# Performance work log

Measured on AMD Instinct MI355X. Metric: run time of the kernel, lower is better.

## Reference

```python
import jax, jax.numpy as jnp
import numpy as np

N_NODES = 50000
N_EDGES = 800000
IN_DIM = 128
HIDDEN = 64
NEG_SLOPE = 0.2


def setup_inputs() -> dict:
    key = jax.random.key(0)
    ks = jax.random.split(key, 8)
    x = jax.random.normal(ks[0], (N_NODES, IN_DIM), dtype=jnp.float32)
    edge_index = jax.random.randint(ks[1], (2, N_EDGES), 0, N_NODES, dtype=jnp.int64)
    # GATConv params (heads=1)
    W = jax.random.normal(ks[2], (HIDDEN, IN_DIM), dtype=jnp.float32) / np.sqrt(IN_DIM)
    att_src = jax.random.normal(ks[3], (HIDDEN,), dtype=jnp.float32) / np.sqrt(HIDDEN)
    att_dst = jax.random.normal(ks[4], (HIDDEN,), dtype=jnp.float32) / np.sqrt(HIDDEN)
    bias_conv = jnp.zeros((HIDDEN,), dtype=jnp.float32)
    # final Linear(hidden, 1)
    W_lin = jax.random.normal(ks[5], (1, HIDDEN), dtype=jnp.float32) / np.sqrt(HIDDEN)
    b_lin = jnp.zeros((1,), dtype=jnp.float32)
    return {"x": x, "edge_index": edge_index, "W": W, "att_src": att_src,
            "att_dst": att_dst, "bias_conv": bias_conv, "W_lin": W_lin, "b_lin": b_lin}


def _gat_forward(x, edge_index, W, att_src, att_dst, bias_conv, W_lin, b_lin):
    n = x.shape[0]
    # add self-loops (PyG GATConv default)
    loop = jnp.arange(n, dtype=edge_index.dtype)
    src = jnp.concatenate([edge_index[0], loop])  # source nodes j (messages from)
    dst = jnp.concatenate([edge_index[1], loop])  # destination nodes i (aggregated at)

    h = x @ W.T                                   # [N, H] projected features
    a_src = h @ att_src                           # [N]
    a_dst = h @ att_dst                           # [N]

    e = jax.nn.leaky_relu(a_src[src] + a_dst[dst], NEG_SLOPE)  # [E']
    # segment softmax over incoming edges of each destination node
    m = jax.ops.segment_max(e, dst, num_segments=n)            # [N]
    ex = jnp.exp(e - m[dst])
    s = jax.ops.segment_sum(ex, dst, num_segments=n)           # [N]
    alpha = ex / s[dst]                                        # [E']

    out = jax.ops.segment_sum(alpha[:, None] * h[src], dst, num_segments=n)
    out = out + bias_conv                         # [N, H]

    out = jax.nn.relu(out)
    # dropout p=0.5 is a no-op in eval mode
    y = jax.nn.sigmoid(out @ W_lin.T + b_lin)     # [N, 1]
    return y


def reference(x, edge_index, W, att_src, att_dst, bias_conv, W_lin, b_lin):
    return _gat_forward(x, edge_index, W, att_src, att_dst, bias_conv, W_lin, b_lin)
```

## Files before the change

kernel.cpp:

```cpp
#include <hip/hip_runtime.h>
#include <hip/hip_bf16.h>
#include <hip/hip_fp16.h>
#include <cstdint>

#define IND 128
#define HID 64
#define NEG_SLOPE 0.2f
#define EPB 4096
#define CBSHIFT 8
#define BCAP 8192
#define SORT_THREADS 256
#define EPT (EPB / SORT_THREADS)

__device__ __forceinline__ unsigned short f2bf_bits(float f) {
  __hip_bfloat16 b = __float2bfloat16(f);
  return *reinterpret_cast<unsigned short*>(&b);
}
__device__ __forceinline__ unsigned short f2h_bits(float f) {
  __half h = __float2half(f);
  return *reinterpret_cast<unsigned short*>(&h);
}
__device__ __forceinline__ float h2f_bits(unsigned short u) {
  __half_raw r; r.x = u;
  return __half2float(__half(r));
}
__device__ __forceinline__ float bf2f_bits(unsigned short u) {
  return __uint_as_float((unsigned)u << 16);
}
__device__ __forceinline__ unsigned pack_bf2(float lo, float hi) {
  return (unsigned)f2bf_bits(lo) | ((unsigned)f2bf_bits(hi) << 16);
}
__device__ __forceinline__ float bf_lo(unsigned u) {
  return __uint_as_float(u << 16);
}
__device__ __forceinline__ float bf_hi(unsigned u) {
  return __uint_as_float(u & 0xFFFF0000u);
}

__global__ __launch_bounds__(256) void k_proj_sort(
    const float* __restrict__ x, const float* __restrict__ W,
    const float* __restrict__ att_s, const float* __restrict__ att_d,
    unsigned short* __restrict__ h, float* __restrict__ a_src,
    float* __restrict__ a_dst,
    const int* __restrict__ ei, int* __restrict__ gcur,
    unsigned* __restrict__ tmp, int E, long long E2,
    int nSort, int nbuck, int n)
{
  __shared__ __align__(16) char smem[49664];
  const int tid = threadIdx.x;

  if (blockIdx.x < (unsigned)nSort) {
    int* hist       = (int*)smem;
    int* sums       = hist + 256;
    int* cur        = sums + 256;
    int* gbase      = cur + 256;
    unsigned* sorted = (unsigned*)(gbase + 256);

    hist[tid] = 0;
    __syncthreads();

    const long long i0 = (long long)blockIdx.x * EPB;

    unsigned pk[EPT];
#pragma unroll
    for (int j = 0; j < EPT; ++j) {
      long long idx = i0 + j * SORT_THREADS + tid;
      unsigned v = 0xFFFFFFFFu;
      if (idx < E2) {
        int s, d;
        if (idx < E) { s = ei[idx]; d = ei[E + idx]; }
        else         { s = d = (int)(idx - E); }
        v = ((unsigned)d << 16) | (unsigned)s;
        atomicAdd(&hist[d >> CBSHIFT], 1);
      }
      pk[j] = v;
    }
    __syncthreads();

    sums[tid] = hist[tid];
    __syncthreads();
    for (int off = 1; off < 256; off <<= 1) {
      int t = (tid >= off) ? sums[tid - off] : 0;
      __syncthreads();
      sums[tid] += t;
      __syncthreads();
    }
    {
      const int lstart_t = sums[tid] - hist[tid];
      cur[tid] = lstart_t;
      gbase[tid] = (tid < nbuck && hist[tid] > 0)
                     ? tid * BCAP + atomicAdd(&gcur[tid], hist[tid]) : 0;
    }
    __syncthreads();
    hist[tid] = sums[tid] - hist[tid];
    __syncthreads();

#pragma unroll
    for (int j = 0; j < EPT; ++j) {
      unsigned v = pk[j];
      if (v != 0xFFFFFFFFu) {
        int b = v >> (16 + CBSHIFT);
        int lpos = atomicAdd(&cur[b], 1);
        sorted[lpos] = v;
      }
    }
    __syncthreads();

    const int cntE = (int)((E2 - i0 < EPB) ? (E2 - i0) : EPB);
    for (int i = tid; i < cntE; i += SORT_THREADS) {
      unsigned v = sorted[i];
      int b = v >> (16 + CBSHIFT);
      tmp[gbase[b] + (i - hist[b])] = v;
    }
    return;
  }

  float*    xs   = (float*)smem;
  unsigned* wt   = (unsigned*)(smem + 32768);
  float*    sa_l = (float*)(smem + 49152);
  float*    sd_l = (float*)(smem + 49408);

  const int nodeBase = (blockIdx.x - nSort) * 64;

  if (tid < 64) { sa_l[tid] = 0.f; sd_l[tid] = 0.f; }

#pragma unroll
  for (int it = 0; it < 4; ++it) {
    int fi = (it * 256 + tid) * 8;
    int row = fi >> 7, k = fi & 127;
    float4 w0 = *(const float4*)(W + fi);
    float4 w1 = *(const float4*)(W + fi + 4);
    uint4 pv;
    pv.x = pack_bf2(w0.x, w0.y);
    pv.y = pack_bf2(w0.z, w0.w);
    pv.z = pack_bf2(w1.x, w1.y);
    pv.w = pack_bf2(w1.z, w1.w);
    int c = (k >> 3) ^ ((row >> 2) & 7);
    ((uint4*)wt)[row * 16 + c] = pv;
  }
#pragma unroll
  for (int it = 0; it < 8; ++it) {
    int fi = (it * 256 + tid) * 4;
    int nl = fi >> 7, k = fi & 127;
    int ks = k ^ (((nl >> 2) & 7) << 2);
    int node = nodeBase + nl; if (node >= n) node = n - 1;
    float4 v = *(const float4*)(x + (size_t)node * IND + k);
    *(float4*)&xs[nl * 128 + ks] = v;
  }
  __syncthreads();

  const int ng = tid & 15;
  const int hg = tid >> 4;
  const int swzA = (ng & 7) << 2;
  const int swzB = hg & 7;
  const float* xrow0 = &xs[(4 * ng) * 128];
  const uint4* wrow0 = ((const uint4*)wt) + (4 * hg) * 16;

  float acc[4][4];
#pragma unroll
  for (int j = 0; j < 4; ++j)
#pragma unroll
    for (int i = 0; i < 4; ++i) acc[j][i] = 0.f;

  for (int k = 0; k < IND; k += 8) {
    float4 a0[4], a1[4];
#pragma unroll
    for (int j = 0; j < 4; ++j) {
      a0[j] = *(const float4*)(xrow0 + j * 128 + (k ^ swzA));
      a1[j] = *(const float4*)(xrow0 + j * 128 + ((k + 4) ^ swzA));
    }
    uint4 bw[4];
#pragma unroll
    for (int i = 0; i < 4; ++i)
      bw[i] = wrow0[i * 16 + ((k >> 3) ^ swzB)];

#pragma unroll
    for (int i = 0; i < 4; ++i) {
      float b0 = bf_lo(bw[i].x), b1 = bf_hi(bw[i].x);
      float b2 = bf_lo(bw[i].y), b3 = bf_hi(bw[i].y);
      float b4 = bf_lo(bw[i].z), b5 = bf_hi(bw[i].z);
      float b6 = bf_lo(bw[i].w), b7 = bf_hi(bw[i].w);
#pragma unroll
      for (int j = 0; j < 4; ++j) {
        acc[j][i] = fmaf(a0[j].x, b0, acc[j][i]);
        acc[j][i] = fmaf(a0[j].y, b1, acc[j][i]);
        acc[j][i] = fmaf(a0[j].z, b2, acc[j][i]);
        acc[j][i] = fmaf(a0[j].w, b3, acc[j][i]);
        acc[j][i] = fmaf(a1[j].x, b4, acc[j][i]);
        acc[j][i] = fmaf(a1[j].y, b5, acc[j][i]);
        acc[j][i] = fmaf(a1[j].z, b6, acc[j][i]);
        acc[j][i] = fmaf(a1[j].w, b7, acc[j][i]);
      }
    }
  }

#pragma unroll
  for (int j = 0; j < 4; ++j) {
    int node = nodeBase + 4 * ng + j;
    if (node < n) {
      ushort4 hv;
      hv.x = f2bf_bits(acc[j][0]);
      hv.y = f2bf_bits(acc[j][1]);
      hv.z = f2bf_bits(acc[j][2]);
      hv.w = f2bf_bits(acc[j][3]);
      *(ushort4*)(h + (size_t)node * HID + 4 * hg) = hv;
    }
  }

  float4 as4 = *(const float4*)(att_s + 4 * hg);
  float4 ad4 = *(const float4*)(att_d + 4 * hg);
#pragma unroll
  for (int j = 0; j < 4; ++j) {
    float ps = acc[j][0]*as4.x + acc[j][1]*as4.y + acc[j][2]*as4.z + acc[j][3]*as4.w;
    float pd = acc[j][0]*ad4.x + acc[j][1]*ad4.y + acc[j][2]*ad4.z + acc[j][3]*ad4.w;
    ps += __shfl_xor(ps, 16, 64); ps += __shfl_xor(ps, 32, 64);
    pd += __shfl_xor(pd, 16, 64); pd += __shfl_xor(pd, 32, 64);
    if ((tid & 63) < 16) {
      atomicAdd(&sa_l[4 * ng + j], ps);
      atomicAdd(&sd_l[4 * ng + j], pd);
    }
  }
  __syncthreads();
  if (tid < 64) {
    int node = nodeBase + tid;
    if (node < n) { a_src[node] = sa_l[tid]; a_dst[node] = sd_l[tid]; }
  }
}

__global__ __launch_bounds__(1024) void k_csr(
    const unsigned* __restrict__ tmp, const int* __restrict__ gcur,
    const float* __restrict__ a_src, const float* __restrict__ a_dst,
    int* __restrict__ row_start, int* __restrict__ deg_out,
    unsigned* __restrict__ csr4, int n, int nbuck)
{
  __shared__ int degl[256], sums[256], cur[256];
  __shared__ float adl[256];

  const int tid = threadIdx.x;
  const int b   = blockIdx.x;
  const int n0  = b << CBSHIFT;
  const int base = b * BCAP;
  const int next = base + gcur[b];

  if (tid < 256) {
    degl[tid] = 0;
    const int node = n0 + tid;
    adl[tid] = (node < n) ? a_dst[node] : 0.f;
  }
  __syncthreads();

  for (int i = base + tid; i < next; i += 1024)
    atomicAdd(&degl[(tmp[i] >> 16) - n0], 1);
  __syncthreads();

  if (tid < 256) sums[tid] = degl[tid];
  __syncthreads();
  for (int off = 1; off < 256; off <<= 1) {
    int t = (tid >= off && tid < 256) ? sums[tid - off] : 0;
    __syncthreads();
    if (tid < 256) sums[tid] += t;
    __syncthreads();
  }
  if (tid < 256) {
    const int rs = base + sums[tid] - degl[tid];
    cur[tid] = rs;
    const int node = n0 + tid;
    if (node < n) { row_start[node] = rs; deg_out[node] = degl[tid]; }
  }
  __syncthreads();

  for (int i = base + tid; i < next; i += 1024) {
    unsigned v = tmp[i];
    int s  = (int)(v & 0xFFFFu);
    int dl = (int)(v >> 16) - n0;
    float sc = a_src[s] + adl[dl];
    sc = (sc >= 0.f) ? sc : NEG_SLOPE * sc;
    float w = expf(sc);
    int pos = atomicAdd(&cur[dl], 1);
    csr4[pos] = (unsigned)s | ((unsigned)f2h_bits(w) << 16);
  }
}

__global__ __launch_bounds__(256) void k_gather_final(
    const int* __restrict__ row_start, const int* __restrict__ deg,
    const unsigned* __restrict__ csr4, const unsigned short* __restrict__ h,
    const float* __restrict__ bias, const float* __restrict__ W_lin,
    const float* __restrict__ b_lin, float* __restrict__ y, int n)
{
  const int lane = threadIdx.x & 63;
  const int wid  = threadIdx.x >> 6;
  const int node = blockIdx.x * 4 + wid;
  if (node >= n) return;

  const int rs = row_start[node];
  const int dg = deg[node];

  const int quarter = lane >> 4;
  const int sub     = lane & 15;

  float wpart = 0.f;
  float acc0 = 0.f, acc1 = 0.f, acc2 = 0.f, acc3 = 0.f;

  for (int b = 0; b < dg; b += 64) {
    int i = b + lane;
    unsigned pk = (i < dg) ? csr4[rs + i] : 0u;
    wpart += h2f_bits((unsigned short)(pk >> 16));
    const int cnt = (dg - b < 64) ? (dg - b) : 64;

    int j = 0;
    for (; j + 8 <= cnt; j += 8) {
#pragma unroll
      for (int g = 0; g < 2; ++g) {
        int e = j + 4 * g + quarter;
        unsigned pe = __shfl(pk, e, 64);
        float we = h2f_bits((unsigned short)(pe >> 16));
        unsigned se = pe & 0xFFFFu;
        ushort4 hb = ((const ushort4*)(h + (size_t)se * HID))[sub];
        acc0 = fmaf(we, bf2f_bits(hb.x), acc0);
        acc1 = fmaf(we, bf2f_bits(hb.y), acc1);
        acc2 = fmaf(we, bf2f_bits(hb.z), acc2);
        acc3 = fmaf(we, bf2f_bits(hb.w), acc3);
      }
    }
    for (; j < cnt; j += 4) {
      int e = j + quarter;
      bool val = e < cnt;
      unsigned pe = __shfl(pk, val ? e : 0, 64);
      float we = val ? h2f_bits((unsigned short)(pe >> 16)) : 0.f;
      unsigned se = val ? (pe & 0xFFFFu) : 0u;
      ushort4 hb = ((const ushort4*)(h + (size_t)se * HID))[sub];
      acc0 = fmaf(we, bf2f_bits(hb.x), acc0);
      acc1 = fmaf(we, bf2f_bits(hb.y), acc1);
      acc2 = fmaf(we, bf2f_bits(hb.z), acc2);
      acc3 = fmaf(we, bf2f_bits(hb.w), acc3);
    }
  }

  acc0 += __shfl_xor(acc0, 16, 64); acc0 += __shfl_xor(acc0, 32, 64);
  acc1 += __shfl_xor(acc1, 16, 64); acc1 += __shfl_xor(acc1, 32, 64);
  acc2 += __shfl_xor(acc2, 16, 64); acc2 += __shfl_xor(acc2, 32, 64);
  acc3 += __shfl_xor(acc3, 16, 64); acc3 += __shfl_xor(acc3, 32, 64);

  float wsum = wpart;
#pragma unroll
  for (int o = 32; o; o >>= 1) wsum += __shfl_xor(wsum, o, 64);
  const float inv = 1.f / wsum;

  float4 bb = ((const float4*)bias)[sub];
  float4 ww = ((const float4*)W_lin)[sub];
  float v0 = fmaxf(acc0 * inv + bb.x, 0.f);
  float v1 = fmaxf(acc1 * inv + bb.y, 0.f);
  float v2 = fmaxf(acc2 * inv + bb.z, 0.f);
  float v3 = fmaxf(acc3 * inv + bb.w, 0.f);
  float z = v0 * ww.x + v1 * ww.y + v2 * ww.z + v3 * ww.w;
#pragma unroll
  for (int o = 8; o; o >>= 1) z += __shfl_xor(z, o, 64);
  if (lane == 0)
    y[node] = 1.f / (1.f + expf(-(z + b_lin[0])));
}


extern "C" void kernel_launch(void* const* d_in, const int* in_sizes, int n_in,
                              void* d_out, int out_size, void* d_ws, size_t ws_size,
                              hipStream_t stream)
{
  const float* x     = (const float*)d_in[0];
  const int*   ei    = (const int*)d_in[1];
  const float* W     = (const float*)d_in[2];
  const float* att_s = (const float*)d_in[3];
  const float* att_d = (const float*)d_in[4];
  const float* bias  = (const float*)d_in[5];
  const float* W_lin = (const float*)d_in[6];
  const float* b_lin = (const float*)d_in[7];
  float* y = (float*)d_out;

  const int n = in_sizes[0] / IND;
  const int E = in_sizes[1] / 2;
  const long long E2 = (long long)E + n;
  const int nSort = (int)((E2 + EPB - 1) / EPB);
  const int nProj = (n + 63) / 64;
  const int nbuck = (n + (1 << CBSHIFT) - 1) >> CBSHIFT;

  char* ws = (char*)d_ws;
  unsigned short* h = (unsigned short*)ws; ws += (size_t)n * HID * sizeof(unsigned short);
  float*    a_src  = (float*)ws;    ws += (size_t)n * sizeof(float);
  float*    a_dst  = (float*)ws;    ws += (size_t)n * sizeof(float);
  int*      row_st = (int*)ws;      ws += (size_t)n * sizeof(int);
  int*      deg    = (int*)ws;      ws += (size_t)n * sizeof(int);
  int*      gcur   = (int*)ws;      ws += (size_t)nbuck * sizeof(int);
  unsigned* tmp    = (unsigned*)ws; ws += (size_t)nbuck * BCAP * sizeof(unsigned);
  unsigned* csr4   = (unsigned*)ws; ws += (size_t)nbuck * BCAP * sizeof(unsigned);

  hipMemsetAsync(gcur, 0, (size_t)nbuck * sizeof(int), stream);

  k_proj_sort<<<nSort + nProj, 256, 0, stream>>>(
      x, W, att_s, att_d, h, a_src, a_dst,
      ei, gcur, tmp, E, E2, nSort, nbuck, n);

  k_csr<<<nbuck, 1024, 0, stream>>>(tmp, gcur, a_src, a_dst, row_st, deg, csr4,
                                    n, nbuck);

  k_gather_final<<<(n + 3) / 4, 256, 0, stream>>>(
      row_st, deg, csr4, h, bias, W_lin, b_lin, y, n);
}
```

Baseline: 141.0 us.

## Fuse CSR build and neighbor gather into one kernel using shared-memory CSR

Merges the CSR construction kernel and the gather/final kernel so each bucket block builds its CSR slice in LDS (32KB) and then its 16 waves process the bucket's 256 destination nodes directly. This removes the global csr4/row_start/deg writes and reads plus one kernel launch. In exchange, parallelism for the gather drops to nbuck (~196) blocks of 1024 threads with high LDS use, which may underfill the GPU during the latency-bound h gathers.

After: 147.0 us. 4.3% more time.

```diff
diff --git a/kernel.cpp b/kernel.cpp
--- a/kernel.cpp
+++ b/kernel.cpp
@@ -227,14 +227,16 @@
   }
 }
 
-__global__ __launch_bounds__(1024) void k_csr(
+__global__ __launch_bounds__(1024) void k_csr_gather(
     const unsigned* __restrict__ tmp, const int* __restrict__ gcur,
     const float* __restrict__ a_src, const float* __restrict__ a_dst,
-    int* __restrict__ row_start, int* __restrict__ deg_out,
-    unsigned* __restrict__ csr4, int n, int nbuck)
+    const unsigned short* __restrict__ h,
+    const float* __restrict__ bias, const float* __restrict__ W_lin,
+    const float* __restrict__ b_lin, float* __restrict__ y, int n)
 {
   __shared__ int degl[256], sums[256], cur[256];
   __shared__ float adl[256];
+  __shared__ unsigned csrw[BCAP];
 
   const int tid = threadIdx.x;
   const int b   = blockIdx.x;
@@ -261,12 +263,7 @@
     if (tid < 256) sums[tid] += t;
     __syncthreads();
   }
-  if (tid < 256) {
-    const int rs = base + sums[tid] - degl[tid];
-    cur[tid] = rs;
-    const int node = n0 + tid;
-    if (node < n) { row_start[node] = rs; deg_out[node] = degl[tid]; }
-  }
+  if (tid < 256) cur[tid] = sums[tid] - degl[tid];
   __syncthreads();
 
   for (int i = base + tid; i < next; i += 1024) {
@@ -277,44 +274,52 @@
     sc = (sc >= 0.f) ? sc : NEG_SLOPE * sc;
     float w = expf(sc);
     int pos = atomicAdd(&cur[dl], 1);
-    csr4[pos] = (unsigned)s | ((unsigned)f2h_bits(w) << 16);
-  }
-}
-
-__global__ __launch_bounds__(256) void k_gather_final(
-    const int* __restrict__ row_start, const int* __restrict__ deg,
-    const unsigned* __restrict__ csr4, const unsigned short* __restrict__ h,
-    const float* __restrict__ bias, const float* __restrict__ W_lin,
-    const float* __restrict__ b_lin, float* __restrict__ y, int n)
-{
-  const int lane = threadIdx.x & 63;
-  const int wid  = threadIdx.x >> 6;
-  const int node = blockIdx.x * 4 + wid;
-  if (node >= n) return;
-
-  const int rs = row_start[node];
-  const int dg = deg[node];
-
+    csrw[pos] = (unsigned)s | ((unsigned)f2h_bits(w) << 16);
+  }
+  __syncthreads();
+
+  const int lane    = tid & 63;
+  const int wid     = tid >> 6;
   const int quarter = lane >> 4;
   const int sub     = lane & 15;
 
-  float wpart = 0.f;
-  float acc0 = 0.f, acc1 = 0.f, acc2 = 0.f, acc3 = 0.f;
-
-  for (int b = 0; b < dg; b += 64) {
-    int i = b + lane;
-    unsigned pk = (i < dg) ? csr4[rs + i] : 0u;
-    wpart += h2f_bits((unsigned short)(pk >> 16));
-    const int cnt = (dg - b < 64) ? (dg - b) : 64;
-
-    int j = 0;
-    for (; j + 8 <= cnt; j += 8) {
-#pragma unroll
-      for (int g = 0; g < 2; ++g) {
-        int e = j + 4 * g + quarter;
-        unsigned pe = __shfl(pk, e, 64);
-        float we = h2f_bits((unsigned short)(pe >> 16));
-        unsigned se = pe & 0xFFFFu;
+  for (int nl = wid; nl < 256; nl += 16) {
+    const int node = n0 + nl;
+    if (node >= n) break;
+
+    const int dg  = degl[nl];
+    const int rsl = sums[nl] - dg;
+
+    float wpart = 0.f;
+    float acc0 = 0.f, acc1 = 0.f, acc2 = 0.f, acc3 = 0.f;
+
+    for (int bb = 0; bb < dg; bb += 64) {
+      int i = bb + lane;
+      unsigned pk = (i < dg) ? csrw[rsl + i] : 0u;
+      wpart += h2f_bits((unsigned short)(pk >> 16));
+      const int cnt = (dg - bb < 64) ? (dg - bb) : 64;
+
+      int j = 0;
+      for (; j + 8 <= cnt; j += 8) {
+#pragma unroll
+        for (int g = 0; g < 2; ++g) {
+          int e = j + 4 * g + quarter;
+          unsigned pe = __shfl(pk, e, 64);
+          float we = h2f_bits((unsigned short)(pe >> 16));
+          unsigned se = pe & 0xFFFFu;
+          ushort4 hb = ((const ushort4*)(h + (size_t)se * HID))[sub];
+          acc0 = fmaf(we, bf2f_bits(hb.x), acc0);
+          acc1 = fmaf(we, bf2f_bits(hb.y), acc1);
+          acc2 = fmaf(we, bf2f_bits(hb.z), acc2);
+          acc3 = fmaf(we, bf2f_bits(hb.w), acc3);
+        }
+      }
+      for (; j < cnt; j += 4) {
+        int e = j + quarter;
+        bool val = e < cnt;
+        unsigned pe = __shfl(pk, val ? e : 0, 64);
+        float we = val ? h2f_bits((unsigned short)(pe >> 16)) : 0.f;
+        unsigned se = val ? (pe & 0xFFFFu) : 0u;
         ushort4 hb = ((const ushort4*)(h + (size_t)se * HID))[sub];
         acc0 = fmaf(we, bf2f_bits(hb.x), acc0);
         acc1 = fmaf(we, bf2f_bits(hb.y), acc1);
@@ -322,41 +327,29 @@
         acc3 = fmaf(we, bf2f_bits(hb.w), acc3);
       }
     }
-    for (; j < cnt; j += 4) {
-      int e = j + quarter;
-      bool val = e < cnt;
-      unsigned pe = __shfl(pk, val ? e : 0, 64);
-      float we = val ? h2f_bits((unsigned short)(pe >> 16)) : 0.f;
-      unsigned se = val ? (pe & 0xFFFFu) : 0u;
-      ushort4 hb = ((const ushort4*)(h + (size_t)se * HID))[sub];
-      acc0 = fmaf(we, bf2f_bits(hb.x), acc0);
-      acc1 = fmaf(we, bf2f_bits(hb.y), acc1);
-      acc2 = fmaf(we, bf2f_bits(hb.z), acc2);
-      acc3 = fmaf(we, bf2f_bits(hb.w), acc3);
-    }
-  }
-
-  acc0 += __shfl_xor(acc0, 16, 64); acc0 += __shfl_xor(acc0, 32, 64);
-  acc1 += __shfl_xor(acc1, 16, 64); acc1 += __shfl_xor(acc1, 32, 64);
-  acc2 += __shfl_xor(acc2, 16, 64); acc2 += __shfl_xor(acc2, 32, 64);
-  acc3 += __shfl_xor(acc3, 16, 64); acc3 += __shfl_xor(acc3, 32, 64);
-
-  float wsum = wpart;
-#pragma unroll
-  for (int o = 32; o; o >>= 1) wsum += __shfl_xor(wsum, o, 64);
-  const float inv = 1.f / wsum;
-
-  float4 bb = ((const float4*)bias)[sub];
-  float4 ww = ((const float4*)W_lin)[sub];
-  float v0 = fmaxf(acc0 * inv + bb.x, 0.f);
-  float v1 = fmaxf(acc1 * inv + bb.y, 0.f);
-  float v2 = fmaxf(acc2 * inv + bb.z, 0.f);
-  float v3 = fmaxf(acc3 * inv + bb.w, 0.f);
-  float z = v0 * ww.x + v1 * ww.y + v2 * ww.z + v3 * ww.w;
-#pragma unroll
-  for (int o = 8; o; o >>= 1) z += __shfl_xor(z, o, 64);
-  if (lane == 0)
-    y[node] = 1.f / (1.f + expf(-(z + b_lin[0])));
+
+    acc0 += __shfl_xor(acc0, 16, 64); acc0 += __shfl_xor(acc0, 32, 64);
+    acc1 += __shfl_xor(acc1, 16, 64); acc1 += __shfl_xor(acc1, 32, 64);
+    acc2 += __shfl_xor(acc2, 16, 64); acc2 += __shfl_xor(acc2, 32, 64);
+    acc3 += __shfl_xor(acc3, 16, 64); acc3 += __shfl_xor(acc3, 32, 64);
+
+    float wsum = wpart;
+#pragma unroll
+    for (int o = 32; o; o >>= 1) wsum += __shfl_xor(wsum, o, 64);
+    const float inv = 1.f / wsum;
+
+    float4 bb4 = ((const float4*)bias)[sub];
+    float4 ww  = ((const float4*)W_lin)[sub];
+    float v0 = fmaxf(acc0 * inv + bb4.x, 0.f);
+    float v1 = fmaxf(acc1 * inv + bb4.y, 0.f);
+    float v2 = fmaxf(acc2 * inv + bb4.z, 0.f);
+    float v3 = fmaxf(acc3 * inv + bb4.w, 0.f);
+    float z = v0 * ww.x + v1 * ww.y + v2 * ww.z + v3 * ww.w;
+#pragma unroll
+    for (int o = 8; o; o >>= 1) z += __shfl_xor(z, o, 64);
+    if (lane == 0)
+      y[node] = 1.f / (1.f + expf(-(z + b_lin[0])));
+  }
 }
 
 
@@ -385,11 +378,8 @@
   unsigned short* h = (unsigned short*)ws; ws += (size_t)n * HID * sizeof(unsigned short);
   float*    a_src  = (float*)ws;    ws += (size_t)n * sizeof(float);
   float*    a_dst  = (float*)ws;    ws += (size_t)n * sizeof(float);
-  int*      row_st = (int*)ws;      ws += (size_t)n * sizeof(int);
-  int*      deg    = (int*)ws;      ws += (size_t)n * sizeof(int);
   int*      gcur   = (int*)ws;      ws += (size_t)nbuck * sizeof(int);
   unsigned* tmp    = (unsigned*)ws; ws += (size_t)nbuck * BCAP * sizeof(unsigned);
-  unsigned* csr4   = (unsigned*)ws; ws += (size_t)nbuck * BCAP * sizeof(unsigned);
 
   hipMemsetAsync(gcur, 0, (size_t)nbuck * sizeof(int), stream);
 
@@ -397,9 +387,6 @@
       x, W, att_s, att_d, h, a_src, a_dst,
       ei, gcur, tmp, E, E2, nSort, nbuck, n);
 
-  k_csr<<<nbuck, 1024, 0, stream>>>(tmp, gcur, a_src, a_dst, row_st, deg, csr4,
-                                    n, nbuck);
-
-  k_gather_final<<<(n + 3) / 4, 256, 0, stream>>>(
-      row_st, deg, csr4, h, bias, W_lin, b_lin, y, n);
-}
+  k_csr_gather<<<nbuck, 1024, 0, stream>>>(
+      tmp, gcur, a_src, a_dst, h, bias, W_lin, b_lin, y, n);
+}
```
